# Optimization experiments

Hardware: AMD Instinct MI355X
Metric: run time of the kernel (lower is better)

Reference implementation:

```python
import jax, jax.numpy as jnp
import numpy as np

B, S, D, H, DH = 4, 2048, 512, 8, 64

def setup_inputs() -> dict:
    key = jax.random.key(0)
    k1, k2, k3, k4 = jax.random.split(key, 4)
    sc = 1.0 / np.sqrt(D)
    return {
        "x": jax.random.normal(k1, (B, S, D), dtype=jnp.float32),
        "Wq": jax.random.normal(k2, (H, D, DH), dtype=jnp.float32) * sc,
        "Wk": jax.random.normal(k3, (H, D, DH), dtype=jnp.float32) * sc,
        "Wv": jax.random.normal(k4, (H, D, DH), dtype=jnp.float32) * sc,
    }

def reference(x, Wq, Wk, Wv):
    # x: [B,S,D]; Wq/Wk/Wv: [H,D,DH] (stacked per-head bias-free Linear weights)
    q = jnp.einsum('bsd,hdk->bhsk', x, Wq)
    k = jnp.einsum('bsd,hdk->bhsk', x, Wk)
    v = jnp.einsum('bsd,hdk->bhsk', x, Wv)
    scale = DH ** -0.5
    scores = jax.nn.softmax(jnp.einsum('bhqk,bhsk->bhqs', q, k) * scale, axis=-1)
    out = jnp.einsum('bhqs,bhsk->bhqk', scores, v)  # [B,H,S,DH]
    # concat heads along last dim (head order matches ModuleList order)
    return out.transpose(0, 2, 1, 3).reshape(B, S, H * DH)
```

## Files before the change

kernel.cpp:

```cpp
#include <hip/hip_runtime.h>

typedef _Float16 half8  __attribute__((ext_vector_type(8)));
typedef _Float16 half4v __attribute__((ext_vector_type(4)));
typedef _Float16 half2v __attribute__((ext_vector_type(2)));
typedef float    float4v __attribute__((ext_vector_type(4)));

#define CSC 0.18033688f

#define WAITV8 asm volatile("s_waitcnt vmcnt(8)" ::: "memory")
#define WAITV0 asm volatile("s_waitcnt vmcnt(0)" ::: "memory")
#define WAITL0 asm volatile("s_waitcnt lgkmcnt(0)" ::: "memory")

__device__ __forceinline__ void async16(const _Float16* g, void* l) {
    __builtin_amdgcn_global_load_lds((const __attribute__((address_space(1))) void*)g,
                                     (__attribute__((address_space(3))) void*)l, 16, 0, 0);
}

__device__ __forceinline__ half2v pk2(float a, float b) {
    return __builtin_bit_cast(half2v, __builtin_amdgcn_cvt_pkrtz(a, b));
}

__global__ __launch_bounds__(256) void mha_prep(const float* __restrict__ x,
    const float* __restrict__ wq, const float* __restrict__ wk, const float* __restrict__ wv,
    _Float16* __restrict__ xh, _Float16* __restrict__ wt) {
    __shared__ __align__(16) _Float16 T[64][72];
    const int tid = threadIdx.x;
    if (blockIdx.x < 4096) {
        int t = blockIdx.x * 256 + tid;
        float4v v = ((const float4v*)x)[t];
        half4v o;
        #pragma unroll
        for (int i = 0; i < 4; ++i) o[i] = (_Float16)v[i];
        ((half4v*)xh)[t] = o;
        return;
    }
    const int blk = blockIdx.x - 4096;
    const int dt = blk & 7, h = (blk >> 3) & 7, mat = blk >> 6;
    const float* w = ((mat == 0) ? wq : (mat == 1) ? wk : wv) + h * 32768 + dt * 64 * 64;
    #pragma unroll
    for (int i = 0; i < 4; ++i) {
        int s = tid + i * 256;
        int dl = s >> 4, c4 = s & 15;
        float4v v = ((const float4v*)(w + (size_t)dl * 64))[c4];
        #pragma unroll
        for (int e = 0; e < 4; ++e) T[c4 * 4 + e][dl] = (_Float16)v[e];
    }
    __syncthreads();
    #pragma unroll
    for (int i = 0; i < 2; ++i) {
        int s = tid + i * 256;
        int dh = s >> 3, c8 = s & 7;
        half8 o;
        #pragma unroll
        for (int e = 0; e < 8; ++e) o[e] = T[dh][c8 * 8 + e];
        *(half8*)(wt + (size_t)((mat * 8 + h) * 64 + dh) * 512 + dt * 64 + c8 * 8) = o;
    }
}

__global__ __launch_bounds__(256, 3) void mha_qkv(const _Float16* __restrict__ xh,
    const _Float16* __restrict__ wt, _Float16* __restrict__ Qm, _Float16* __restrict__ Km,
    _Float16* __restrict__ Vt) {
    __shared__ __align__(16) char smem[34816];
    _Float16* Ash[2] = { (_Float16*)smem,           (_Float16*)(smem + 8192)  };
    _Float16* Bsh[2] = { (_Float16*)(smem + 16384), (_Float16*)(smem + 24576) };
    const int tid = threadIdx.x;
    const int lane = tid & 63, wave = tid >> 6;
    const int quad = lane >> 4, li = lane & 15;
    const int m0 = blockIdx.x * 128, n0 = blockIdx.y * 128;
    float4v acc[4][4] = {};
    const int r0 = tid >> 2, c0 = (tid & 3) ^ ((r0 >> 1) & 3);
    const int s1 = 256 + tid, r1 = s1 >> 2, c1 = (s1 & 3) ^ ((r1 >> 1) & 3);
    const _Float16* gA0 = xh + (size_t)(m0 + r0) * 512 + c0 * 8;
    const _Float16* gA1 = xh + (size_t)(m0 + r1) * 512 + c1 * 8;
    const _Float16* gB0 = wt + (size_t)(n0 + r0) * 512 + c0 * 8;
    const _Float16* gB1 = wt + (size_t)(n0 + r1) * 512 + c1 * 8;
    const int wr = (wave >> 1) * 64, wc = (wave & 1) * 64;
    const char* aB[2]; const char* bB[2];
    #pragma unroll
    for (int bb = 0; bb < 2; ++bb) {
        aB[bb] = (const char*)Ash[bb] + (wr + li) * 64 + ((quad ^ ((li >> 1) & 3)) << 4);
        bB[bb] = (const char*)Bsh[bb] + (wc + li) * 64 + ((quad ^ ((li >> 1) & 3)) << 4);
    }
    auto stage = [&](int bb, int kk) {
        async16(gA0 + kk, (char*)Ash[bb] + wave * 1024);
        async16(gA1 + kk, (char*)Ash[bb] + 4096 + wave * 1024);
        async16(gB0 + kk, (char*)Bsh[bb] + wave * 1024);
        async16(gB1 + kk, (char*)Bsh[bb] + 4096 + wave * 1024);
    };
    auto compute = [&](int bb) {
        half8 af[4], bf[4];
        #pragma unroll
        for (int mt = 0; mt < 4; ++mt) af[mt] = *(const half8*)(aB[bb] + mt * 1024);
        #pragma unroll
        for (int nt = 0; nt < 4; ++nt) bf[nt] = *(const half8*)(bB[bb] + nt * 1024);
        #pragma unroll
        for (int mt = 0; mt < 4; ++mt)
            #pragma unroll
            for (int nt = 0; nt < 4; ++nt)
                acc[mt][nt] = __builtin_amdgcn_mfma_f32_16x16x32_f16(af[mt], bf[nt], acc[mt][nt], 0, 0, 0);
    };
    stage(0, 0);
    for (int kk = 0; kk < 512; kk += 64) {
        __syncthreads();
        stage(1, kk + 32);
        compute(0);
        __syncthreads();
        if (kk + 64 < 512) stage(0, kk + 64);
        compute(1);
    }
    const int mat = n0 >> 9;
    if (mat == 2) {
        #pragma unroll
        for (int mt = 0; mt < 4; ++mt) {
            int m = m0 + wr + mt * 16 + quad * 4;
            int b = m >> 11, s = m & 2047;
            #pragma unroll
            for (int nt = 0; nt < 4; ++nt) {
                int n = n0 + wc + nt * 16 + li;
                int h = (n >> 6) & 7, dh = n & 63;
                int bh = b * 8 + h;
                half4v pkv;
                #pragma unroll
                for (int r = 0; r < 4; ++r) pkv[r] = (_Float16)acc[mt][nt][r];
                *(half4v*)(Vt + ((size_t)bh * 64 + dh) * 2048 + s) = pkv;
            }
        }
    } else {
        _Float16* dst = (mat == 0) ? Qm : Km;
        const float osc = (mat == 0) ? CSC : 1.0f;
        __syncthreads();
        char* Tb = smem;
        #pragma unroll
        for (int mt = 0; mt < 4; ++mt) {
            int rbase = wr + mt * 16 + quad * 4;
            #pragma unroll
            for (int nt = 0; nt < 4; ++nt) {
                int col = wc + nt * 16 + li;
                #pragma unroll
                for (int r = 0; r < 4; ++r)
                    *(_Float16*)(Tb + (rbase + r) * 272 + col * 2) = (_Float16)(acc[mt][nt][r] * osc);
            }
        }
        __syncthreads();
        const int h0 = (n0 >> 6) & 7;
        #pragma unroll
        for (int i = 0; i < 8; ++i) {
            int c = i * 256 + tid;
            int row = c >> 4, j8 = c & 15;
            half8 v = *(const half8*)(Tb + row * 272 + j8 * 16);
            int m = m0 + row;
            int b = m >> 11, s = m & 2047;
            int bh = b * 8 + h0 + (j8 >> 3);
            *(half8*)(dst + ((size_t)bh * 2048 + s) * 64 + (j8 & 7) * 8) = v;
        }
    }
}

__global__ __launch_bounds__(256, 2) void mha_attn(const _Float16* __restrict__ Qm,
    const _Float16* __restrict__ Km, const _Float16* __restrict__ Vt, float* __restrict__ out) {
    __shared__ __align__(16) char smem[65536];
    const int tid = threadIdx.x, lane = tid & 63, wave = tid >> 6;
    const int quad = lane >> 4, li = lane & 15;
    const int strm = wave & 1, hh = wave >> 1;
    const int flat = blockIdx.x;
    const int qb = (flat >> 3) & 15;
    const int bh = ((flat >> 7) << 3) | (flat & 7);
    const int b = bh >> 3, h = bh & 7;
    const _Float16* Qg = Qm + (size_t)bh * 2048 * 64;
    const _Float16* Kg = Km + (size_t)bh * 2048 * 64 + (size_t)strm * 1024 * 64;
    const _Float16* Vg = Vt + (size_t)bh * 64 * 2048 + (size_t)strm * 1024;
    const int q0 = qb * 128 + hh * 64;
    half8 qf[4][2];
    #pragma unroll
    for (int qt = 0; qt < 4; ++qt)
        #pragma unroll
        for (int ds = 0; ds < 2; ++ds)
            qf[qt][ds] = *(const half8*)(Qg + (size_t)(q0 + qt * 16 + li) * 64 + ds * 32 + quad * 8);
    WAITV0;
    half8 vone;
    #pragma unroll
    for (int e = 0; e < 8; ++e) vone[e] = (_Float16)1.0f;
    float4v O[4][4] = {};
    float4v O4[4] = {};
    const int ls = lane >> 3, l7 = lane & 7;
    const _Float16* pKe[2]; const _Float16* pKo[2]; const _Float16* pV[2];
    pKe[0] = Kg + ls * 64 + ((l7 ^ (ls & 3)) << 3);
    pKo[0] = Kg + (ls + 8) * 64 + (((l7 ^ (ls & 3)) ^ 4) << 3);
    const int gsl = l7 ^ ls;
    pV[0] = Vg + (size_t)(ls + ((gsl >> 2) << 5)) * 2048 + ((gsl & 3) << 3);
    pKe[1] = pKe[0] + 2048;  pKo[1] = pKo[0] + 2048;  pV[1] = pV[0] + 32;
    char* const base = smem + wave * 16384;
    char* const dstK[2] = { base,        base + 8192  };
    char* const dstV[2] = { base + 4096, base + 12288 };
    const int rowE = ((li >> 2) << 3) | (li & 3);
    const int swzE = (li & 3) | (((li >> 2) & 1) << 2);
    const char *k0e[2], *k1e[2], *vB[2];
    #pragma unroll
    for (int bb = 0; bb < 2; ++bb) {
        k0e[bb] = dstK[bb] + rowE * 128 + ((quad ^ swzE) << 4);
        k1e[bb] = dstK[bb] + rowE * 128 + (((quad + 4) ^ swzE) << 4);
        vB[bb]  = dstV[bb] + li * 128;
    }
    const int cV0 = (quad ^ (li & 7)) << 4;
    const int cV1 = ((4 + quad) ^ (li & 7)) << 4;
    auto stage = [&](int bb) {
        async16(pKe[bb],         dstK[bb]);
        async16(pKo[bb],         dstK[bb] + 1024);
        async16(pKe[bb] + 1024,  dstK[bb] + 2048);
        async16(pKo[bb] + 1024,  dstK[bb] + 3072);
        async16(pV[bb],          dstV[bb]);
        async16(pV[bb] + 16384,  dstV[bb] + 1024);
        async16(pV[bb] + 32768,  dstV[bb] + 2048);
        async16(pV[bb] + 49152,  dstV[bb] + 3072);
        pKe[bb] += 4096; pKo[bb] += 4096; pV[bb] += 64;
    };
    auto tile = [&](int bb, bool doStage) {
        half8 f0e = *(const half8*)(k0e[bb]);
        half8 f1e = *(const half8*)(k1e[bb]);
        half8 f0o = *(const half8*)(k0e[bb] + 512);
        half8 f1o = *(const half8*)(k1e[bb] + 512);
        half8 vf0 = *(const half8*)(vB[bb] + cV0);
        half8 vf1 = *(const half8*)(vB[bb] + 2048 + cV0);
        half8 vf2 = *(const half8*)(vB[bb] + cV1);
        half8 vf3 = *(const half8*)(vB[bb] + 2048 + cV1);
        WAITL0;
        if (doStage) stage(bb);
        half8 pf[4];
        #pragma unroll
        for (int qt = 0; qt < 4; ++qt) {
            float4v se = {}, so = {};
            __builtin_amdgcn_s_setprio(1);
            se = __builtin_amdgcn_mfma_f32_16x16x32_f16(f0e, qf[qt][0], se, 0, 0, 0);
            se = __builtin_amdgcn_mfma_f32_16x16x32_f16(f1e, qf[qt][1], se, 0, 0, 0);
            so = __builtin_amdgcn_mfma_f32_16x16x32_f16(f0o, qf[qt][0], so, 0, 0, 0);
            so = __builtin_amdgcn_mfma_f32_16x16x32_f16(f1o, qf[qt][1], so, 0, 0, 0);
            __builtin_amdgcn_s_setprio(0);
            float pe[4], po[4];
            #pragma unroll
            for (int r = 0; r < 4; ++r) {
                pe[r] = __builtin_amdgcn_exp2f(se[r]);
                po[r] = __builtin_amdgcn_exp2f(so[r]);
            }
            half4v a = __builtin_shufflevector(pk2(pe[0], pe[1]), pk2(pe[2], pe[3]), 0, 1, 2, 3);
            half4v o = __builtin_shufflevector(pk2(po[0], po[1]), pk2(po[2], po[3]), 0, 1, 2, 3);
            pf[qt] = __builtin_shufflevector(a, o, 0, 1, 2, 3, 4, 5, 6, 7);
        }
        __builtin_amdgcn_s_setprio(1);
        #pragma unroll
        for (int qt = 0; qt < 4; ++qt)
            O4[qt] = __builtin_amdgcn_mfma_f32_16x16x32_f16(pf[qt], vone, O4[qt], 0, 0, 0);
        #pragma unroll
        for (int qt = 0; qt < 4; ++qt) {
            O[qt][0] = __builtin_amdgcn_mfma_f32_16x16x32_f16(pf[qt], vf0, O[qt][0], 0, 0, 0);
            O[qt][1] = __builtin_amdgcn_mfma_f32_16x16x32_f16(pf[qt], vf1, O[qt][1], 0, 0, 0);
            O[qt][2] = __builtin_amdgcn_mfma_f32_16x16x32_f16(pf[qt], vf2, O[qt][2], 0, 0, 0);
            O[qt][3] = __builtin_amdgcn_mfma_f32_16x16x32_f16(pf[qt], vf3, O[qt][3], 0, 0, 0);
        }
        __builtin_amdgcn_s_setprio(0);
    };
    stage(0);
    stage(1);
    #pragma unroll 1
    for (int tp = 0; tp < 15; ++tp) {
        WAITV8; tile(0, true);
        WAITV8; tile(1, true);
    }
    WAITV8; tile(0, false);
    WAITV0; tile(1, false);
    __syncthreads();
    float* Obuf = (float*)smem;
    float* Lbuf = (float*)(smem + 32768);
    if (strm == 1) {
        #pragma unroll
        for (int qt = 0; qt < 4; ++qt) {
            #pragma unroll
            for (int dt = 0; dt < 4; ++dt)
                ((float4v*)(Obuf + hh * 4096))[(qt * 4 + dt) * 64 + lane] = O[qt][dt];
            ((float4v*)(Lbuf + hh * 1024))[qt * 64 + lane] = O4[qt];
        }
    }
    __syncthreads();
    if (strm == 1) return;
    #pragma unroll
    for (int qt = 0; qt < 4; ++qt) {
        #pragma unroll
        for (int dt = 0; dt < 4; ++dt) {
            float4v o2 = ((float4v*)(Obuf + hh * 4096))[(qt * 4 + dt) * 64 + lane];
            O[qt][dt] += o2;
        }
        float4v l2 = ((float4v*)(Lbuf + hh * 1024))[qt * 64 + lane];
        O4[qt] += l2;
    }
    #pragma unroll
    for (int qt = 0; qt < 4; ++qt) {
        #pragma unroll
        for (int r = 0; r < 4; ++r) {
            float inv = 1.0f / O4[qt][r];
            int q = q0 + qt * 16 + quad * 4 + r;
            float* orow = out + ((size_t)(b * 2048 + q)) * 512 + h * 64;
            #pragma unroll
            for (int dt = 0; dt < 4; ++dt) orow[dt * 16 + li] = O[qt][dt][r] * inv;
        }
    }
}

extern "C" void kernel_launch(void* const* d_in, const int* in_sizes, int n_in,
                              void* d_out, int out_size, void* d_ws, size_t ws_size,
                              hipStream_t stream) {
    const float* x  = (const float*)d_in[0];
    const float* wq = (const float*)d_in[1];
    const float* wk = (const float*)d_in[2];
    const float* wv = (const float*)d_in[3];
    float* out = (float*)d_out;
    char* ws = (char*)d_ws;
    _Float16* xh = (_Float16*)(ws);
    _Float16* wt = (_Float16*)(ws + 8388608);
    _Float16* Qm = (_Float16*)(ws + 9961472);
    _Float16* Km = (_Float16*)(ws + 18350080);
    _Float16* Vt = (_Float16*)(ws + 26738688);
    if (ws_size < 35127296u) return;
    mha_prep<<<4288, 256, 0, stream>>>(x, wq, wk, wv, xh, wt);
    mha_qkv<<<dim3(64, 12), 256, 0, stream>>>(xh, wt, Qm, Km, Vt);
    mha_attn<<<512, 256, 0, stream>>>(Qm, Km, Vt, out);
}
```

Baseline: 136.5 us.

## Halve attention query tile, load V directly from global, raise occupancy

The attention kernel now gives each block 64 queries instead of 128 and launches 1024 blocks in place of 512. It cuts LDS to about 33KB and raises launch bounds to 4 blocks per CU. V fragments are read straight from global memory into registers rather than staged through LDS, so only K is double-buffered with async LDS loads and the wait counts change to match. The aim is more resident waves to hide memory latency, at the cost of re-reading K/V twice as often per head and possible uncoalesced V loads.

```diff
diff --git a/kernel.cpp b/kernel.cpp
--- a/kernel.cpp
+++ b/kernel.cpp
@@ -7,7 +7,7 @@
 
 #define CSC 0.18033688f
 
-#define WAITV8 asm volatile("s_waitcnt vmcnt(8)" ::: "memory")
+#define WAITV4 asm volatile("s_waitcnt vmcnt(4)" ::: "memory")
 #define WAITV0 asm volatile("s_waitcnt vmcnt(0)" ::: "memory")
 #define WAITL0 asm volatile("s_waitcnt lgkmcnt(0)" ::: "memory")
 
@@ -156,23 +156,23 @@
     }
 }
 
-__global__ __launch_bounds__(256, 2) void mha_attn(const _Float16* __restrict__ Qm,
+__global__ __launch_bounds__(256, 4) void mha_attn(const _Float16* __restrict__ Qm,
     const _Float16* __restrict__ Km, const _Float16* __restrict__ Vt, float* __restrict__ out) {
-    __shared__ __align__(16) char smem[65536];
+    __shared__ __align__(16) char smem[33280];
     const int tid = threadIdx.x, lane = tid & 63, wave = tid >> 6;
     const int quad = lane >> 4, li = lane & 15;
     const int strm = wave & 1, hh = wave >> 1;
     const int flat = blockIdx.x;
-    const int qb = (flat >> 3) & 15;
-    const int bh = ((flat >> 7) << 3) | (flat & 7);
-    const int b = bh >> 3, h = bh & 7;
+    const int h = flat & 7, rr = flat >> 3;
+    const int qg = rr & 31, b = rr >> 5;
+    const int bh = b * 8 + h;
     const _Float16* Qg = Qm + (size_t)bh * 2048 * 64;
     const _Float16* Kg = Km + (size_t)bh * 2048 * 64 + (size_t)strm * 1024 * 64;
     const _Float16* Vg = Vt + (size_t)bh * 64 * 2048 + (size_t)strm * 1024;
-    const int q0 = qb * 128 + hh * 64;
-    half8 qf[4][2];
-    #pragma unroll
-    for (int qt = 0; qt < 4; ++qt)
+    const int q0 = qg * 64 + hh * 32;
+    half8 qf[2][2];
+    #pragma unroll
+    for (int qt = 0; qt < 2; ++qt)
         #pragma unroll
         for (int ds = 0; ds < 2; ++ds)
             qf[qt][ds] = *(const half8*)(Qg + (size_t)(q0 + qt * 16 + li) * 64 + ds * 32 + quad * 8);
@@ -180,54 +180,45 @@
     half8 vone;
     #pragma unroll
     for (int e = 0; e < 8; ++e) vone[e] = (_Float16)1.0f;
-    float4v O[4][4] = {};
-    float4v O4[4] = {};
+    float4v O[2][4] = {};
+    float4v O4[2] = {};
     const int ls = lane >> 3, l7 = lane & 7;
-    const _Float16* pKe[2]; const _Float16* pKo[2]; const _Float16* pV[2];
-    pKe[0] = Kg + ls * 64 + ((l7 ^ (ls & 3)) << 3);
-    pKo[0] = Kg + (ls + 8) * 64 + (((l7 ^ (ls & 3)) ^ 4) << 3);
-    const int gsl = l7 ^ ls;
-    pV[0] = Vg + (size_t)(ls + ((gsl >> 2) << 5)) * 2048 + ((gsl & 3) << 3);
-    pKe[1] = pKe[0] + 2048;  pKo[1] = pKo[0] + 2048;  pV[1] = pV[0] + 32;
-    char* const base = smem + wave * 16384;
-    char* const dstK[2] = { base,        base + 8192  };
-    char* const dstV[2] = { base + 4096, base + 12288 };
+    const _Float16* pKe = Kg + ls * 64 + ((l7 ^ (ls & 3)) << 3);
+    const _Float16* pKo = Kg + (ls + 8) * 64 + (((l7 ^ (ls & 3)) ^ 4) << 3);
+    char* const base = smem + wave * 8192;
+    char* const dstK[2] = { base, base + 4096 };
     const int rowE = ((li >> 2) << 3) | (li & 3);
     const int swzE = (li & 3) | (((li >> 2) & 1) << 2);
-    const char *k0e[2], *k1e[2], *vB[2];
+    const char* k0e[2]; const char* k1e[2];
     #pragma unroll
     for (int bb = 0; bb < 2; ++bb) {
         k0e[bb] = dstK[bb] + rowE * 128 + ((quad ^ swzE) << 4);
         k1e[bb] = dstK[bb] + rowE * 128 + (((quad + 4) ^ swzE) << 4);
-        vB[bb]  = dstV[bb] + li * 128;
-    }
-    const int cV0 = (quad ^ (li & 7)) << 4;
-    const int cV1 = ((4 + quad) ^ (li & 7)) << 4;
-    auto stage = [&](int bb) {
-        async16(pKe[bb],         dstK[bb]);
-        async16(pKo[bb],         dstK[bb] + 1024);
-        async16(pKe[bb] + 1024,  dstK[bb] + 2048);
-        async16(pKo[bb] + 1024,  dstK[bb] + 3072);
-        async16(pV[bb],          dstV[bb]);
-        async16(pV[bb] + 16384,  dstV[bb] + 1024);
-        async16(pV[bb] + 32768,  dstV[bb] + 2048);
-        async16(pV[bb] + 49152,  dstV[bb] + 3072);
-        pKe[bb] += 4096; pKo[bb] += 4096; pV[bb] += 64;
+    }
+    auto stageK = [&](int bb, int t) {
+        const _Float16* pe = pKe + t * 2048;
+        const _Float16* po = pKo + t * 2048;
+        async16(pe,        dstK[bb]);
+        async16(po,        dstK[bb] + 1024);
+        async16(pe + 1024, dstK[bb] + 2048);
+        async16(po + 1024, dstK[bb] + 3072);
     };
-    auto tile = [&](int bb, bool doStage) {
+    const _Float16* vBase = Vg + (size_t)li * 2048 + quad * 8;
+    auto tile = [&](int bb, int t, bool st) {
+        half8 vf0 = *(const half8*)(vBase + t * 32);
+        half8 vf1 = *(const half8*)(vBase + 32768 + t * 32);
+        half8 vf2 = *(const half8*)(vBase + 65536 + t * 32);
+        half8 vf3 = *(const half8*)(vBase + 98304 + t * 32);
         half8 f0e = *(const half8*)(k0e[bb]);
         half8 f1e = *(const half8*)(k1e[bb]);
         half8 f0o = *(const half8*)(k0e[bb] + 512);
         half8 f1o = *(const half8*)(k1e[bb] + 512);
-        half8 vf0 = *(const half8*)(vB[bb] + cV0);
-        half8 vf1 = *(const half8*)(vB[bb] + 2048 + cV0);
-        half8 vf2 = *(const half8*)(vB[bb] + cV1);
-        half8 vf3 = *(const half8*)(vB[bb] + 2048 + cV1);
         WAITL0;
-        if (doStage) stage(bb);
-        half8 pf[4];
-        #pragma unroll
-        for (int qt = 0; qt < 4; ++qt) {
+        if (st) stageK(bb, t + 2);
+        WAITV4;
+        half8 pf[2];
+        #pragma unroll
+        for (int qt = 0; qt < 2; ++qt) {
             float4v se = {}, so = {};
             __builtin_amdgcn_s_setprio(1);
             se = __builtin_amdgcn_mfma_f32_16x16x32_f16(f0e, qf[qt][0], se, 0, 0, 0);
@@ -247,10 +238,10 @@
         }
         __builtin_amdgcn_s_setprio(1);
         #pragma unroll
-        for (int qt = 0; qt < 4; ++qt)
+        for (int qt = 0; qt < 2; ++qt)
             O4[qt] = __builtin_amdgcn_mfma_f32_16x16x32_f16(pf[qt], vone, O4[qt], 0, 0, 0);
         #pragma unroll
-        for (int qt = 0; qt < 4; ++qt) {
+        for (int qt = 0; qt < 2; ++qt) {
             O[qt][0] = __builtin_amdgcn_mfma_f32_16x16x32_f16(pf[qt], vf0, O[qt][0], 0, 0, 0);
             O[qt][1] = __builtin_amdgcn_mfma_f32_16x16x32_f16(pf[qt], vf1, O[qt][1], 0, 0, 0);
             O[qt][2] = __builtin_amdgcn_mfma_f32_16x16x32_f16(pf[qt], vf2, O[qt][2], 0, 0, 0);
@@ -258,41 +249,47 @@
         }
         __builtin_amdgcn_s_setprio(0);
     };
-    stage(0);
-    stage(1);
+    stageK(0, 0);
+    stageK(1, 1);
+    WAITV4;
     #pragma unroll 1
-    for (int tp = 0; tp < 15; ++tp) {
-        WAITV8; tile(0, true);
-        WAITV8; tile(1, true);
-    }
-    WAITV8; tile(0, false);
-    WAITV0; tile(1, false);
+    for (int i = 0; i < 15; ++i) {
+        tile(0, 2 * i,     true);
+        tile(1, 2 * i + 1, true);
+    }
+    tile(0, 30, false);
+    tile(1, 31, false);
     __syncthreads();
-    float* Obuf = (float*)smem;
-    float* Lbuf = (float*)(smem + 32768);
+    float* Ob = (float*)smem;
+    float* Lb = (float*)(smem + 32768);
     if (strm == 1) {
         #pragma unroll
-        for (int qt = 0; qt < 4; ++qt) {
+        for (int qt = 0; qt < 2; ++qt) {
             #pragma unroll
             for (int dt = 0; dt < 4; ++dt)
-                ((float4v*)(Obuf + hh * 4096))[(qt * 4 + dt) * 64 + lane] = O[qt][dt];
-            ((float4v*)(Lbuf + hh * 1024))[qt * 64 + lane] = O4[qt];
+                ((float4v*)(Ob + hh * 2048))[(qt * 4 + dt) * 64 + lane] = O[qt][dt];
+            if (li == 0) {
+                #pragma unroll
+                for (int r = 0; r < 4; ++r)
+                    Lb[hh * 32 + qt * 16 + quad * 4 + r] = O4[qt][r];
+            }
         }
     }
     __syncthreads();
     if (strm == 1) return;
     #pragma unroll
-    for (int qt = 0; qt < 4; ++qt) {
+    for (int qt = 0; qt < 2; ++qt) {
         #pragma unroll
         for (int dt = 0; dt < 4; ++dt) {
-            float4v o2 = ((float4v*)(Obuf + hh * 4096))[(qt * 4 + dt) * 64 + lane];
+            float4v o2 = ((float4v*)(Ob + hh * 2048))[(qt * 4 + dt) * 64 + lane];
             O[qt][dt] += o2;
         }
-        float4v l2 = ((float4v*)(Lbuf + hh * 1024))[qt * 64 + lane];
-        O4[qt] += l2;
-    }
-    #pragma unroll
-    for (int qt = 0; qt < 4; ++qt) {
+        #pragma unroll
+        for (int r = 0; r < 4; ++r)
+            O4[qt][r] += Lb[hh * 32 + qt * 16 + quad * 4 + r];
+    }
+    #pragma unroll
+    for (int qt = 0; qt < 2; ++qt) {
         #pragma unroll
         for (int r = 0; r < 4; ++r) {
             float inv = 1.0f / O4[qt][r];
@@ -321,5 +318,5 @@
     if (ws_size < 35127296u) return;
     mha_prep<<<4288, 256, 0, stream>>>(x, wq, wk, wv, xh, wt);
     mha_qkv<<<dim3(64, 12), 256, 0, stream>>>(xh, wt, Qm, Km, Vt);
-    mha_attn<<<512, 256, 0, stream>>>(Qm, Km, Vt, out);
-}
+    mha_attn<<<1024, 256, 0, stream>>>(Qm, Km, Vt, out);
+}
```

Result: slower. 176.7 us (+29.5%).

## Software-pipeline QK^T MFMAs of the next tile with exp/PV of the previous

Applied to the files above, without the earlier changes.

Splits the per-tile body into a QK-score phase and a finish phase (exp2, packing, PV and row-sum MFMAs). The loop is then interleaved so the score MFMAs for one buffer are issued before the softmax and PV work for the other buffer. The aim is to hide transcendental and conversion latency behind independent matrix work. The cost is that scores and V fragments for two tiles stay live at once, which raises VGPR pressure and could reduce occupancy or cause spills.

```diff
diff --git a/kernel.cpp b/kernel.cpp
--- a/kernel.cpp
+++ b/kernel.cpp
@@ -214,32 +214,38 @@
         async16(pV[bb] + 49152,  dstV[bb] + 3072);
         pKe[bb] += 4096; pKo[bb] += 4096; pV[bb] += 64;
     };
-    auto tile = [&](int bb, bool doStage) {
+    auto qkphase = [&](int bb, bool doStage, float4v sE[4], float4v sO[4], half8 vf[4]) {
         half8 f0e = *(const half8*)(k0e[bb]);
         half8 f1e = *(const half8*)(k1e[bb]);
         half8 f0o = *(const half8*)(k0e[bb] + 512);
         half8 f1o = *(const half8*)(k1e[bb] + 512);
-        half8 vf0 = *(const half8*)(vB[bb] + cV0);
-        half8 vf1 = *(const half8*)(vB[bb] + 2048 + cV0);
-        half8 vf2 = *(const half8*)(vB[bb] + cV1);
-        half8 vf3 = *(const half8*)(vB[bb] + 2048 + cV1);
+        vf[0] = *(const half8*)(vB[bb] + cV0);
+        vf[1] = *(const half8*)(vB[bb] + 2048 + cV0);
+        vf[2] = *(const half8*)(vB[bb] + cV1);
+        vf[3] = *(const half8*)(vB[bb] + 2048 + cV1);
         WAITL0;
         if (doStage) stage(bb);
-        half8 pf[4];
+        __builtin_amdgcn_s_setprio(1);
         #pragma unroll
         for (int qt = 0; qt < 4; ++qt) {
             float4v se = {}, so = {};
-            __builtin_amdgcn_s_setprio(1);
             se = __builtin_amdgcn_mfma_f32_16x16x32_f16(f0e, qf[qt][0], se, 0, 0, 0);
             se = __builtin_amdgcn_mfma_f32_16x16x32_f16(f1e, qf[qt][1], se, 0, 0, 0);
             so = __builtin_amdgcn_mfma_f32_16x16x32_f16(f0o, qf[qt][0], so, 0, 0, 0);
             so = __builtin_amdgcn_mfma_f32_16x16x32_f16(f1o, qf[qt][1], so, 0, 0, 0);
-            __builtin_amdgcn_s_setprio(0);
+            sE[qt] = se; sO[qt] = so;
+        }
+        __builtin_amdgcn_s_setprio(0);
+    };
+    auto finish = [&](const float4v sE[4], const float4v sO[4], const half8 vf[4]) {
+        half8 pf[4];
+        #pragma unroll
+        for (int qt = 0; qt < 4; ++qt) {
             float pe[4], po[4];
             #pragma unroll
             for (int r = 0; r < 4; ++r) {
-                pe[r] = __builtin_amdgcn_exp2f(se[r]);
-                po[r] = __builtin_amdgcn_exp2f(so[r]);
+                pe[r] = __builtin_amdgcn_exp2f(sE[qt][r]);
+                po[r] = __builtin_amdgcn_exp2f(sO[qt][r]);
             }
             half4v a = __builtin_shufflevector(pk2(pe[0], pe[1]), pk2(pe[2], pe[3]), 0, 1, 2, 3);
             half4v o = __builtin_shufflevector(pk2(po[0], po[1]), pk2(po[2], po[3]), 0, 1, 2, 3);
@@ -251,22 +257,32 @@
             O4[qt] = __builtin_amdgcn_mfma_f32_16x16x32_f16(pf[qt], vone, O4[qt], 0, 0, 0);
         #pragma unroll
         for (int qt = 0; qt < 4; ++qt) {
-            O[qt][0] = __builtin_amdgcn_mfma_f32_16x16x32_f16(pf[qt], vf0, O[qt][0], 0, 0, 0);
-            O[qt][1] = __builtin_amdgcn_mfma_f32_16x16x32_f16(pf[qt], vf1, O[qt][1], 0, 0, 0);
-            O[qt][2] = __builtin_amdgcn_mfma_f32_16x16x32_f16(pf[qt], vf2, O[qt][2], 0, 0, 0);
-            O[qt][3] = __builtin_amdgcn_mfma_f32_16x16x32_f16(pf[qt], vf3, O[qt][3], 0, 0, 0);
+            O[qt][0] = __builtin_amdgcn_mfma_f32_16x16x32_f16(pf[qt], vf[0], O[qt][0], 0, 0, 0);
+            O[qt][1] = __builtin_amdgcn_mfma_f32_16x16x32_f16(pf[qt], vf[1], O[qt][1], 0, 0, 0);
+            O[qt][2] = __builtin_amdgcn_mfma_f32_16x16x32_f16(pf[qt], vf[2], O[qt][2], 0, 0, 0);
+            O[qt][3] = __builtin_amdgcn_mfma_f32_16x16x32_f16(pf[qt], vf[3], O[qt][3], 0, 0, 0);
         }
         __builtin_amdgcn_s_setprio(0);
     };
+    float4v sEa[4], sOa[4], sEb[4], sOb[4];
+    half8 vA[4], vBv[4];
     stage(0);
     stage(1);
+    WAITV8;
+    qkphase(0, true, sEa, sOa, vA);
     #pragma unroll 1
-    for (int tp = 0; tp < 15; ++tp) {
-        WAITV8; tile(0, true);
-        WAITV8; tile(1, true);
-    }
-    WAITV8; tile(0, false);
-    WAITV0; tile(1, false);
+    for (int i = 0; i < 15; ++i) {
+        WAITV8;
+        qkphase(1, true, sEb, sOb, vBv);
+        finish(sEa, sOa, vA);
+        WAITV8;
+        qkphase(0, i < 14, sEa, sOa, vA);
+        finish(sEb, sOb, vBv);
+    }
+    WAITV0;
+    qkphase(1, false, sEb, sOb, vBv);
+    finish(sEa, sOa, vA);
+    finish(sEb, sOb, vBv);
     __syncthreads();
     float* Obuf = (float*)smem;
     float* Lbuf = (float*)(smem + 32768);
```

New measurement: 139.8 us. 2.4% more time.

## Restructure KV pipeline to load both buffers then stage both ahead

Applied to the files above, without the earlier changes.

The loop now waits for all outstanding global-to-LDS loads and reads both K/V buffers into registers at once. It then issues staging for both next tiles before computing the two tiles back to back, replacing the alternating double-buffer scheme with per-tile vmcnt(8) waits. The aim is fewer wait points and a longer stretch of MFMA work to hide the global loads behind. In exchange, each iteration fully drains the load queue and holds twice as many fragment registers live, which can raise register pressure and expose load latency at the start of each iteration.

```diff
diff --git a/kernel.cpp b/kernel.cpp
--- a/kernel.cpp
+++ b/kernel.cpp
@@ -7,7 +7,6 @@
 
 #define CSC 0.18033688f
 
-#define WAITV8 asm volatile("s_waitcnt vmcnt(8)" ::: "memory")
 #define WAITV0 asm volatile("s_waitcnt vmcnt(0)" ::: "memory")
 #define WAITL0 asm volatile("s_waitcnt lgkmcnt(0)" ::: "memory")
 
@@ -214,17 +213,8 @@
         async16(pV[bb] + 49152,  dstV[bb] + 3072);
         pKe[bb] += 4096; pKo[bb] += 4096; pV[bb] += 64;
     };
-    auto tile = [&](int bb, bool doStage) {
-        half8 f0e = *(const half8*)(k0e[bb]);
-        half8 f1e = *(const half8*)(k1e[bb]);
-        half8 f0o = *(const half8*)(k0e[bb] + 512);
-        half8 f1o = *(const half8*)(k1e[bb] + 512);
-        half8 vf0 = *(const half8*)(vB[bb] + cV0);
-        half8 vf1 = *(const half8*)(vB[bb] + 2048 + cV0);
-        half8 vf2 = *(const half8*)(vB[bb] + cV1);
-        half8 vf3 = *(const half8*)(vB[bb] + 2048 + cV1);
-        WAITL0;
-        if (doStage) stage(bb);
+    auto computeT = [&](half8 f0e, half8 f1e, half8 f0o, half8 f1o,
+                        half8 vf0, half8 vf1, half8 vf2, half8 vf3) {
         half8 pf[4];
         #pragma unroll
         for (int qt = 0; qt < 4; ++qt) {
@@ -261,12 +251,29 @@
     stage(0);
     stage(1);
     #pragma unroll 1
-    for (int tp = 0; tp < 15; ++tp) {
-        WAITV8; tile(0, true);
-        WAITV8; tile(1, true);
-    }
-    WAITV8; tile(0, false);
-    WAITV0; tile(1, false);
+    for (int p = 0; p < 16; ++p) {
+        WAITV0;
+        half8 fA0e = *(const half8*)(k0e[0]);
+        half8 fA1e = *(const half8*)(k1e[0]);
+        half8 fA0o = *(const half8*)(k0e[0] + 512);
+        half8 fA1o = *(const half8*)(k1e[0] + 512);
+        half8 vA0  = *(const half8*)(vB[0] + cV0);
+        half8 vA1  = *(const half8*)(vB[0] + 2048 + cV0);
+        half8 vA2  = *(const half8*)(vB[0] + cV1);
+        half8 vA3  = *(const half8*)(vB[0] + 2048 + cV1);
+        half8 fB0e = *(const half8*)(k0e[1]);
+        half8 fB1e = *(const half8*)(k1e[1]);
+        half8 fB0o = *(const half8*)(k0e[1] + 512);
+        half8 fB1o = *(const half8*)(k1e[1] + 512);
+        half8 vB0  = *(const half8*)(vB[1] + cV0);
+        half8 vB1  = *(const half8*)(vB[1] + 2048 + cV0);
+        half8 vB2  = *(const half8*)(vB[1] + cV1);
+        half8 vB3  = *(const half8*)(vB[1] + 2048 + cV1);
+        WAITL0;
+        if (p < 15) { stage(0); stage(1); }
+        computeT(fA0e, fA1e, fA0o, fA1o, vA0, vA1, vA2, vA3);
+        computeT(fB0e, fB1e, fB0o, fB1o, vB0, vB1, vB2, vB3);
+    }
     __syncthreads();
     float* Obuf = (float*)smem;
     float* Lbuf = (float*)(smem + 32768);
```

Result: no change. 137.3 us (+0.6%).
